# Kernel tuning notes

Hardware: AMD Instinct MI355X
Metric: run time of the kernel (lower is better)

## Reference

```python
import jax, jax.numpy as jnp
import numpy as np

C = 256
NUM_HEADS = 8
GROUPS = 8
EPS = 1e-5


def setup_inputs() -> dict:
    key = jax.random.key(0)
    ks = jax.random.split(key, 7)
    B, H, W = 2, 64, 64
    x = jax.random.normal(ks[0], (B, C, H, W), dtype=jnp.float32)
    gn_weight = jnp.ones((C,), dtype=jnp.float32)
    gn_bias = jnp.zeros((C,), dtype=jnp.float32)
    # 1x1 convs == per-pixel linear layers
    w_qkv = jax.random.normal(ks[1], (3 * C, C), dtype=jnp.float32) * (1.0 / np.sqrt(C))
    b_qkv = jax.random.normal(ks[2], (3 * C,), dtype=jnp.float32) * 0.01
    w_proj = jax.random.normal(ks[3], (C, C), dtype=jnp.float32) * (1.0 / np.sqrt(C))
    b_proj = jax.random.normal(ks[4], (C,), dtype=jnp.float32) * 0.01
    return {"x": x, "gn_weight": gn_weight, "gn_bias": gn_bias,
            "w_qkv": w_qkv, "b_qkv": b_qkv, "w_proj": w_proj, "b_proj": b_proj}


def reference(x, gn_weight, gn_bias, w_qkv, b_qkv, w_proj, b_proj):
    B, Cc, H, W = x.shape
    nh = NUM_HEADS
    hd = Cc // nh
    N = H * W
    scale = hd ** (-0.5)

    # GroupNorm(8, C): normalize over (C/G, H, W) per group, biased variance
    xg = x.reshape(B, GROUPS, Cc // GROUPS, H, W)
    mean = xg.mean(axis=(2, 3, 4), keepdims=True)
    var = xg.var(axis=(2, 3, 4), keepdims=True)
    hn = (xg - mean) * jax.lax.rsqrt(var + EPS)
    hn = hn.reshape(B, Cc, H, W) * gn_weight[None, :, None, None] + gn_bias[None, :, None, None]

    hf = hn.reshape(B, Cc, N)                       # [B, C, N]
    qkv = jnp.einsum('oc,bcn->bon', w_qkv, hf) + b_qkv[None, :, None]  # [B, 3C, N]
    qkv = qkv.reshape(B, 3, nh, hd, N)
    # q,k,v: [B, nh, N, hd]
    q = jnp.transpose(qkv[:, 0], (0, 1, 3, 2))
    k = jnp.transpose(qkv[:, 1], (0, 1, 3, 2))
    v = jnp.transpose(qkv[:, 2], (0, 1, 3, 2))

    attn = jnp.einsum('bhqd,bhkd->bhqk', q, k) * scale  # [B, nh, N, N]
    attn = jax.nn.softmax(attn, axis=-1)
    o = jnp.einsum('bhqk,bhkd->bhqd', attn, v)           # [B, nh, N, hd]
    o = jnp.transpose(o, (0, 1, 3, 2)).reshape(B, Cc, H, W)

    of = o.reshape(B, Cc, N)
    out = jnp.einsum('oc,bcn->bon', w_proj, of) + b_proj[None, :, None]
    return out.reshape(B, Cc, H, W)
```

## Files before the change

kernel.cpp:

```cpp
#include <hip/hip_runtime.h>


typedef _Float16 half8 __attribute__((ext_vector_type(8)));
typedef __fp16   fp16x2 __attribute__((ext_vector_type(2)));
typedef float    f32x4 __attribute__((ext_vector_type(4)));
typedef int      int2v __attribute__((ext_vector_type(2)));
typedef int      int4v __attribute__((ext_vector_type(4)));

__device__ __forceinline__ f32x4 mfma16(half8 a, half8 b, f32x4 c) {
  return __builtin_amdgcn_mfma_f32_16x16x32_f16(a, b, c, 0, 0, 0);
}

#if __has_builtin(__builtin_amdgcn_exp2f)
#define EXP2(x) __builtin_amdgcn_exp2f(x)
#else
#define EXP2(x) exp2f(x)
#endif

__device__ __forceinline__ unsigned short h_bits(_Float16 h) {
  return __builtin_bit_cast(unsigned short, h);
}
__device__ __forceinline__ int h2_bits(fp16x2 h) {
  return __builtin_bit_cast(int, h);
}

constexpr float CSCALE = (float)(1.4426950408889634 / 5.656854249492381);
constexpr float VSCALE = 0.0009765625f;
constexpr float VUNSC  = 1024.0f;

__global__ __launch_bounds__(256) void prep(const float* __restrict__ x,
                                            float* __restrict__ stats,
                                            const float* __restrict__ wq,
                                            const float* __restrict__ wp,
                                            _Float16* __restrict__ wqh,
                                            _Float16* __restrict__ wph) {
  const int tid = threadIdx.x;
  if (blockIdx.x < 512) {
    const int bg = blockIdx.x >> 5, ch = blockIdx.x & 31;
    const float* p = x + (size_t)bg * 131072 + (size_t)ch * 4096;
    float s = 0.f, ss = 0.f;
#pragma unroll
    for (int j = 0; j < 4; ++j) {
      f32x4 v = *(const f32x4*)(p + j * 1024 + tid * 4);
#pragma unroll
      for (int k = 0; k < 4; ++k) { s += v[k]; ss += v[k] * v[k]; }
    }
#pragma unroll
    for (int m = 1; m <= 32; m <<= 1) { s += __shfl_xor(s, m); ss += __shfl_xor(ss, m); }
    __shared__ float red[8];
    const int wv = tid >> 6;
    if ((tid & 63) == 0) { red[wv * 2] = s; red[wv * 2 + 1] = ss; }
    __syncthreads();
    if (tid == 0) {
      float S = red[0] + red[2] + red[4] + red[6];
      float SS = red[1] + red[3] + red[5] + red[7];
      atomicAdd(&stats[bg * 2], S);
      atomicAdd(&stats[bg * 2 + 1], SS);
    }
  } else {
    const int idx = (blockIdx.x - 512) * 256 + tid;
    if (idx < 196608) {
      wqh[idx] = (_Float16)wq[idx];
    } else {
      wph[idx - 196608] = (_Float16)wp[idx - 196608];
    }
  }
}

__global__ __launch_bounds__(256) void gn_apply(const float* __restrict__ x,
                                                const float* __restrict__ gw,
                                                const float* __restrict__ gb,
                                                const float* __restrict__ stats,
                                                _Float16* __restrict__ hn) {
  __shared__ float tile[64 * 65];
  const int tid = threadIdx.x;
  const int a = tid & 15;
  const int row16 = tid >> 4;
  const int b = blockIdx.z, c0 = blockIdx.y * 64, n0 = blockIdx.x * 64;
#pragma unroll
  for (int m = 0; m < 4; ++m) {
    const int cl = row16 + 16 * m;
    const int c = c0 + cl;
    const int g = c >> 5;
    const float s = stats[(b * 8 + g) * 2];
    const float ss = stats[(b * 8 + g) * 2 + 1];
    const float mean = s * (1.f / 131072.f);
    const float var = ss * (1.f / 131072.f) - mean * mean;
    const float rstd = rsqrtf(var + 1e-5f);
    const float ga = gw[c] * rstd;
    const float be = gb[c] - mean * ga;
    f32x4 xv = *(const f32x4*)(x + ((size_t)(b * 256 + c)) * 4096 + n0 + a * 4);
#pragma unroll
    for (int j = 0; j < 4; ++j) tile[cl * 65 + a * 4 + j] = xv[j] * ga + be;
  }
  __syncthreads();
#pragma unroll
  for (int m = 0; m < 4; ++m) {
    const int nl = row16 + 16 * m;
    const int cb = a * 4;
    int2v uh;
    unsigned short hh[4];
#pragma unroll
    for (int j = 0; j < 4; ++j) {
      hh[j] = h_bits((_Float16)tile[(cb + j) * 65 + nl]);
    }
    uh[0] = hh[0] | (hh[1] << 16); uh[1] = hh[2] | (hh[3] << 16);
    size_t off = ((size_t)(b * 4096 + n0 + nl)) * 256 + c0 + cb;
    *(int2v*)(hn + off) = uh;
  }
}

template <int MODE>
__global__ __launch_bounds__(256) void gemm_f16(
    const _Float16* __restrict__ W, const _Float16* __restrict__ Bm,
    const float* __restrict__ bias,
    _Float16* __restrict__ qkT, _Float16* __restrict__ v_t,
    float* __restrict__ outp) {
  __shared__ _Float16 a_lds[2][4096];
  __shared__ _Float16 b_lds[2][4096];
  const int tid = threadIdx.x, lane = tid & 63, wv = tid >> 6;
  const int qq = lane >> 4, ii = lane & 15;
  const int m0 = blockIdx.x * 64, n0 = blockIdx.y * 64, bz = blockIdx.z;

  const _Float16* asrc[2];
  const _Float16* bsrc[2];
  int dst8[2];
#pragma unroll
  for (int rep = 0; rep < 2; ++rep) {
    const int idx = tid + 256 * rep;
    dst8[rep] = idx * 8;
    const int j = idx >> 7, c = (idx >> 6) & 1, l = idx & 63;
    const int lq = l >> 4, li = l & 15;
    asrc[rep] = W + (size_t)(m0 + 16 * j + li) * 256 + 32 * c + 8 * lq;
    bsrc[rep] = Bm + ((size_t)(bz * 4096 + n0 + 16 * j + li)) * 256 + 32 * c + 8 * lq;
  }

  f32x4 acc[4] = {};

  half8 ar0 = *(const half8*)asrc[0];
  half8 ar1 = *(const half8*)asrc[1];
  half8 br0 = *(const half8*)bsrc[0];
  half8 br1 = *(const half8*)bsrc[1];
  *(half8*)(a_lds[0] + dst8[0]) = ar0;
  *(half8*)(a_lds[0] + dst8[1]) = ar1;
  *(half8*)(b_lds[0] + dst8[0]) = br0;
  *(half8*)(b_lds[0] + dst8[1]) = br1;
  __syncthreads();

  for (int it = 0; it < 4; ++it) {
    const int cur = it & 1;
    if (it < 3) {
      const int ko = (it + 1) * 64;
      ar0 = *(const half8*)(asrc[0] + ko);
      ar1 = *(const half8*)(asrc[1] + ko);
      br0 = *(const half8*)(bsrc[0] + ko);
      br1 = *(const half8*)(bsrc[1] + ko);
    }
    half8 ah0 = *(const half8*)(a_lds[cur] + ((wv * 2 + 0) * 64 + lane) * 8);
    half8 ah1 = *(const half8*)(a_lds[cur] + ((wv * 2 + 1) * 64 + lane) * 8);
#pragma unroll
    for (int t = 0; t < 4; ++t) {
      half8 b0 = *(const half8*)(b_lds[cur] + ((t * 2 + 0) * 64 + lane) * 8);
      half8 b1 = *(const half8*)(b_lds[cur] + ((t * 2 + 1) * 64 + lane) * 8);
      acc[t] = mfma16(ah0, b0, acc[t]);
      acc[t] = mfma16(ah1, b1, acc[t]);
    }
    if (it < 3) {
      _Float16* an = a_lds[cur ^ 1];
      _Float16* bn = b_lds[cur ^ 1];
      *(half8*)(an + dst8[0]) = ar0;
      *(half8*)(an + dst8[1]) = ar1;
      *(half8*)(bn + dst8[0]) = br0;
      *(half8*)(bn + dst8[1]) = br1;
    }
    __syncthreads();
  }

  const int och0 = m0 + 16 * wv + 4 * qq;
  if (MODE == 0) {
    if (m0 < 512) {
      const float sc = (m0 < 256) ? CSCALE : 1.0f;
#pragma unroll
      for (int t = 0; t < 4; ++t) {
        const int n = n0 + 16 * t + ii;
        unsigned short hh[4];
#pragma unroll
        for (int r = 0; r < 4; ++r) {
          hh[r] = h_bits((_Float16)((acc[t][r] + bias[och0 + r]) * sc));
        }
        int2v u;
        u[0] = hh[0] | (hh[1] << 16);
        u[1] = hh[2] | (hh[3] << 16);
        *(int2v*)(qkT + ((size_t)(bz * 4096 + n)) * 512 + och0) = u;
      }
    } else {
#pragma unroll
      for (int t = 0; t < 4; ++t) {
#pragma unroll
        for (int r = 0; r < 4; ++r) {
          const int och = och0 + r;
          const int d = och - 512;
          const int hd_ = d & 31, head = d >> 5;
          const int n = n0 + 16 * t + ii;
          v_t[((size_t)((bz * 8 + head) * 32 + hd_)) * 4096 + n] =
              (_Float16)((acc[t][r] + bias[och]) * VSCALE);
        }
      }
    }
  } else {
#pragma unroll
    for (int t = 0; t < 4; ++t) {
#pragma unroll
      for (int r = 0; r < 4; ++r) {
        const int och = och0 + r;
        const int n = n0 + 16 * t + ii;
        outp[((size_t)(bz * 256 + och)) * 4096 + n] = acc[t][r] + bias[och];
      }
    }
  }
}

__global__ __launch_bounds__(256, 8) void attn_kernel(
    const _Float16* __restrict__ qkT, const _Float16* __restrict__ v_t,
    _Float16* __restrict__ opart, float* __restrict__ lpart, int pbase) {
  __shared__ _Float16 k_lds[2][2048];
  __shared__ _Float16 v_lds[2][2048];
  const int tid = threadIdx.x, lane = tid & 63, wv = tid >> 6;
  const int qq = lane >> 4, ii = lane & 15;
  const int bh = blockIdx.y, b = bh >> 3, h = bh & 7;
  const int n0 = blockIdx.x * 128;
  const int part = pbase + blockIdx.z;
  const int key0 = part * 512;

  const _Float16* qbase =
      qkT + ((size_t)(b * 4096 + n0 + 32 * wv + ii)) * 512 + h * 32 + 8 * qq;
  half8 qf0 = *(const half8*)qbase;
  half8 qf1 = *(const half8*)(qbase + (size_t)16 * 512);

  const int f = tid >> 6, l = tid & 63;
  const int fq = l >> 4, fi = l & 15;
  const int u0 = f >> 1, hf = f & 1;
  const int g = 32 * u0 + 4 * hf + 8 * (fi >> 2) + (fi & 3);
  const _Float16* ksrc =
      qkT + ((size_t)(b * 4096 + key0 + g)) * 512 + 256 + h * 32 + 8 * fq;
  const _Float16* vsrc =
      v_t + ((size_t)(bh * 32 + 16 * hf + fi)) * 4096 + key0 + 32 * u0 + 8 * fq;
  const int dst8 = tid * 8;

  half8 ones8;
#pragma unroll
  for (int j = 0; j < 8; ++j) ones8[j] = (_Float16)1.0f;

  f32x4 o00 = {}, o10 = {}, o01 = {}, o11 = {}, accl0 = {}, accl1 = {};

  half8 kr = *(const half8*)ksrc;
  half8 vr = *(const half8*)vsrc;
  *(half8*)(k_lds[0] + dst8) = kr;
  *(half8*)(v_lds[0] + dst8) = vr;
  __syncthreads();

  for (int kb = 0; kb < 8; ++kb) {
    const int cur = kb & 1;
    if (kb < 7) {
      kr = *(const half8*)(ksrc + (size_t)(kb + 1) * 64 * 512);
      vr = *(const half8*)(vsrc + (size_t)(kb + 1) * 64);
    }
    const _Float16* kbase = k_lds[cur];
    const _Float16* vbase = v_lds[cur];

#pragma unroll
    for (int u = 0; u < 2; ++u) {
      half8 kfa = *(const half8*)(kbase + u * 1024 + lane * 8);
      half8 kfb = *(const half8*)(kbase + u * 1024 + 512 + lane * 8);
      f32x4 z = {};
      f32x4 sa0 = mfma16(kfa, qf0, z);
      f32x4 sb0 = mfma16(kfb, qf0, z);
      f32x4 sa1 = mfma16(kfa, qf1, z);
      f32x4 sb1 = mfma16(kfb, qf1, z);
      int4v p0, p1;
      p0[0] = h2_bits(__builtin_amdgcn_cvt_pkrtz(EXP2(sa0[0]), EXP2(sa0[1])));
      p0[1] = h2_bits(__builtin_amdgcn_cvt_pkrtz(EXP2(sa0[2]), EXP2(sa0[3])));
      p0[2] = h2_bits(__builtin_amdgcn_cvt_pkrtz(EXP2(sb0[0]), EXP2(sb0[1])));
      p0[3] = h2_bits(__builtin_amdgcn_cvt_pkrtz(EXP2(sb0[2]), EXP2(sb0[3])));
      p1[0] = h2_bits(__builtin_amdgcn_cvt_pkrtz(EXP2(sa1[0]), EXP2(sa1[1])));
      p1[1] = h2_bits(__builtin_amdgcn_cvt_pkrtz(EXP2(sa1[2]), EXP2(sa1[3])));
      p1[2] = h2_bits(__builtin_amdgcn_cvt_pkrtz(EXP2(sb1[0]), EXP2(sb1[1])));
      p1[3] = h2_bits(__builtin_amdgcn_cvt_pkrtz(EXP2(sb1[2]), EXP2(sb1[3])));
      half8 pt0 = __builtin_bit_cast(half8, p0);
      half8 pt1 = __builtin_bit_cast(half8, p1);
      half8 vf0 = *(const half8*)(vbase + u * 1024 + lane * 8);
      half8 vf1 = *(const half8*)(vbase + u * 1024 + 512 + lane * 8);
      o00 = mfma16(vf0, pt0, o00);
      o10 = mfma16(vf1, pt0, o10);
      accl0 = mfma16(ones8, pt0, accl0);
      o01 = mfma16(vf0, pt1, o01);
      o11 = mfma16(vf1, pt1, o11);
      accl1 = mfma16(ones8, pt1, accl1);
    }

    if (kb < 7) {
      *(half8*)(k_lds[cur ^ 1] + dst8) = kr;
      *(half8*)(v_lds[cur ^ 1] + dst8) = vr;
    }
    __syncthreads();
  }

#pragma unroll
  for (int hfq = 0; hfq < 2; ++hfq) {
    const f32x4 oa = hfq ? o01 : o00;
    const f32x4 ob = hfq ? o11 : o10;
    const int q = n0 + 32 * wv + 16 * hfq + ii;
    _Float16* base =
        opart + ((size_t)((part * 2 + b) * 4096 + q)) * 256 + h * 32;
    unsigned short hh[4];
    int2v ua;
#pragma unroll
    for (int r = 0; r < 4; ++r) hh[r] = h_bits((_Float16)oa[r]);
    ua[0] = hh[0] | (hh[1] << 16); ua[1] = hh[2] | (hh[3] << 16);
    *(int2v*)(base + 4 * qq) = ua;
#pragma unroll
    for (int r = 0; r < 4; ++r) hh[r] = h_bits((_Float16)ob[r]);
    ua[0] = hh[0] | (hh[1] << 16); ua[1] = hh[2] | (hh[3] << 16);
    *(int2v*)(base + 16 + 4 * qq) = ua;
    if (qq == 0) {
      lpart[((size_t)((part * 2 + b) * 4096 + q)) * 8 + h] =
          hfq ? accl1[0] : accl0[0];
    }
  }
}

__global__ __launch_bounds__(256) void attn_combine(
    const _Float16* __restrict__ opart, const float* __restrict__ lpart,
    _Float16* __restrict__ o16) {
  const int c = threadIdx.x, hh = c >> 5;
#pragma unroll
  for (int k = 0; k < 4; ++k) {
    const int row = blockIdx.x * 4 + k;
    const int b = row >> 12, q = row & 4095;
    float O = 0.f, L = 0.f;
#pragma unroll
    for (int p = 0; p < 8; ++p) {
      O += (float)opart[((size_t)((p * 2 + b) * 4096 + q)) * 256 + c];
      L += lpart[((size_t)((p * 2 + b) * 4096 + q)) * 8 + hh];
    }
    o16[(size_t)row * 256 + c] = (_Float16)(O * (VUNSC / L));
  }
}

extern "C" void kernel_launch(void* const* d_in, const int* in_sizes, int n_in,
                              void* d_out, int out_size, void* d_ws, size_t ws_size,
                              hipStream_t stream) {
  const float* x     = (const float*)d_in[0];
  const float* gnw   = (const float*)d_in[1];
  const float* gnb   = (const float*)d_in[2];
  const float* wqkv  = (const float*)d_in[3];
  const float* bqkv  = (const float*)d_in[4];
  const float* wproj = (const float*)d_in[5];
  const float* bproj = (const float*)d_in[6];
  float* out = (float*)d_out;

  char* ws = (char*)d_ws;
  size_t off = 0;
  auto alloc = [&](size_t bytes) -> char* {
    char* p = ws + off;
    off += (bytes + 255) & ~(size_t)255;
    return p;
  };
  float*    stats  = (float*)alloc(128);
  _Float16* hn     = (_Float16*)alloc((size_t)2 * 4096 * 256 * 2);
  _Float16* wq_h   = (_Float16*)alloc((size_t)768 * 256 * 2);
  _Float16* wp_h   = (_Float16*)alloc((size_t)256 * 256 * 2);
  _Float16* qkT    = (_Float16*)alloc((size_t)2 * 4096 * 512 * 2);
  _Float16* v_t    = (_Float16*)alloc((size_t)16 * 32 * 4096 * 2);
  _Float16* opart  = (_Float16*)alloc((size_t)16 * 4096 * 256 * 2);
  float*    lpart  = (float*)alloc((size_t)16 * 4096 * 8 * 4);
  _Float16* o16 = hn;
  if (off > ws_size) return;

  (void)hipMemsetAsync(stats, 0, 256, stream);
  prep<<<1536, 256, 0, stream>>>(x, stats, wqkv, wproj, wq_h, wp_h);
  gn_apply<<<dim3(64, 4, 2), 256, 0, stream>>>(x, gnw, gnb, stats, hn);
  gemm_f16<0><<<dim3(12, 64, 2), 256, 0, stream>>>(wq_h, hn, bqkv, qkT, v_t,
                                                   nullptr);
  attn_kernel<<<dim3(32, 16, 4), 256, 0, stream>>>(qkT, v_t, opart, lpart, 0);
  attn_kernel<<<dim3(32, 16, 4), 256, 0, stream>>>(qkT, v_t, opart, lpart, 4);
  attn_combine<<<2048, 256, 0, stream>>>(opart, lpart, o16);
  gemm_f16<1><<<dim3(4, 64, 2), 256, 0, stream>>>(wp_h, o16, bproj, nullptr,
                                                  nullptr, out);
}
```

Before: 185.6 us.

## Halve attention key splits and fuse partial combine into projection GEMM

The attention key split goes from 8 partitions of 512 keys over two launches to 4 partitions of 1024 keys in one launch, which halves the partial-output traffic. The separate combine kernel is replaced by a tiny kernel that reduces row sums to inverse normalisers. The projection GEMM now sums the 4 fp16 partials and scales them while staging its B operand. This removes one launch and one full intermediate write and read, at the cost of longer attention blocks, fewer concurrent blocks, and partial summation done in fp16.

```diff
diff --git a/kernel.cpp b/kernel.cpp
--- a/kernel.cpp
+++ b/kernel.cpp
@@ -110,12 +110,10 @@
   }
 }
 
-template <int MODE>
-__global__ __launch_bounds__(256) void gemm_f16(
+__global__ __launch_bounds__(256) void gemm_qkv(
     const _Float16* __restrict__ W, const _Float16* __restrict__ Bm,
     const float* __restrict__ bias,
-    _Float16* __restrict__ qkT, _Float16* __restrict__ v_t,
-    float* __restrict__ outp) {
+    _Float16* __restrict__ qkT, _Float16* __restrict__ v_t) {
   __shared__ _Float16 a_lds[2][4096];
   __shared__ _Float16 b_lds[2][4096];
   const int tid = threadIdx.x, lane = tid & 63, wv = tid >> 6;
@@ -177,35 +175,20 @@
   }
 
   const int och0 = m0 + 16 * wv + 4 * qq;
-  if (MODE == 0) {
-    if (m0 < 512) {
-      const float sc = (m0 < 256) ? CSCALE : 1.0f;
-#pragma unroll
-      for (int t = 0; t < 4; ++t) {
-        const int n = n0 + 16 * t + ii;
-        unsigned short hh[4];
-#pragma unroll
-        for (int r = 0; r < 4; ++r) {
-          hh[r] = h_bits((_Float16)((acc[t][r] + bias[och0 + r]) * sc));
-        }
-        int2v u;
-        u[0] = hh[0] | (hh[1] << 16);
-        u[1] = hh[2] | (hh[3] << 16);
-        *(int2v*)(qkT + ((size_t)(bz * 4096 + n)) * 512 + och0) = u;
+  if (m0 < 512) {
+    const float sc = (m0 < 256) ? CSCALE : 1.0f;
+#pragma unroll
+    for (int t = 0; t < 4; ++t) {
+      const int n = n0 + 16 * t + ii;
+      unsigned short hh[4];
+#pragma unroll
+      for (int r = 0; r < 4; ++r) {
+        hh[r] = h_bits((_Float16)((acc[t][r] + bias[och0 + r]) * sc));
       }
-    } else {
-#pragma unroll
-      for (int t = 0; t < 4; ++t) {
-#pragma unroll
-        for (int r = 0; r < 4; ++r) {
-          const int och = och0 + r;
-          const int d = och - 512;
-          const int hd_ = d & 31, head = d >> 5;
-          const int n = n0 + 16 * t + ii;
-          v_t[((size_t)((bz * 8 + head) * 32 + hd_)) * 4096 + n] =
-              (_Float16)((acc[t][r] + bias[och]) * VSCALE);
-        }
-      }
+      int2v u;
+      u[0] = hh[0] | (hh[1] << 16);
+      u[1] = hh[2] | (hh[3] << 16);
+      *(int2v*)(qkT + ((size_t)(bz * 4096 + n)) * 512 + och0) = u;
     }
   } else {
 #pragma unroll
@@ -213,8 +196,11 @@
 #pragma unroll
       for (int r = 0; r < 4; ++r) {
         const int och = och0 + r;
+        const int d = och - 512;
+        const int hd_ = d & 31, head = d >> 5;
         const int n = n0 + 16 * t + ii;
-        outp[((size_t)(bz * 256 + och)) * 4096 + n] = acc[t][r] + bias[och];
+        v_t[((size_t)((bz * 8 + head) * 32 + hd_)) * 4096 + n] =
+            (_Float16)((acc[t][r] + bias[och]) * VSCALE);
       }
     }
   }
@@ -222,15 +208,15 @@
 
 __global__ __launch_bounds__(256, 8) void attn_kernel(
     const _Float16* __restrict__ qkT, const _Float16* __restrict__ v_t,
-    _Float16* __restrict__ opart, float* __restrict__ lpart, int pbase) {
+    _Float16* __restrict__ opart, float* __restrict__ lpart) {
   __shared__ _Float16 k_lds[2][2048];
   __shared__ _Float16 v_lds[2][2048];
   const int tid = threadIdx.x, lane = tid & 63, wv = tid >> 6;
   const int qq = lane >> 4, ii = lane & 15;
   const int bh = blockIdx.y, b = bh >> 3, h = bh & 7;
   const int n0 = blockIdx.x * 128;
-  const int part = pbase + blockIdx.z;
-  const int key0 = part * 512;
+  const int part = blockIdx.z;
+  const int key0 = part * 1024;
 
   const _Float16* qbase =
       qkT + ((size_t)(b * 4096 + n0 + 32 * wv + ii)) * 512 + h * 32 + 8 * qq;
@@ -259,9 +245,9 @@
   *(half8*)(v_lds[0] + dst8) = vr;
   __syncthreads();
 
-  for (int kb = 0; kb < 8; ++kb) {
+  for (int kb = 0; kb < 16; ++kb) {
     const int cur = kb & 1;
-    if (kb < 7) {
+    if (kb < 15) {
       kr = *(const half8*)(ksrc + (size_t)(kb + 1) * 64 * 512);
       vr = *(const half8*)(vsrc + (size_t)(kb + 1) * 64);
     }
@@ -298,7 +284,7 @@
       accl1 = mfma16(ones8, pt1, accl1);
     }
 
-    if (kb < 7) {
+    if (kb < 15) {
       *(half8*)(k_lds[cur ^ 1] + dst8) = kr;
       *(half8*)(v_lds[cur ^ 1] + dst8) = vr;
     }
@@ -329,21 +315,103 @@
   }
 }
 
-__global__ __launch_bounds__(256) void attn_combine(
-    const _Float16* __restrict__ opart, const float* __restrict__ lpart,
-    _Float16* __restrict__ o16) {
-  const int c = threadIdx.x, hh = c >> 5;
-#pragma unroll
-  for (int k = 0; k < 4; ++k) {
-    const int row = blockIdx.x * 4 + k;
-    const int b = row >> 12, q = row & 4095;
-    float O = 0.f, L = 0.f;
-#pragma unroll
-    for (int p = 0; p < 8; ++p) {
-      O += (float)opart[((size_t)((p * 2 + b) * 4096 + q)) * 256 + c];
-      L += lpart[((size_t)((p * 2 + b) * 4096 + q)) * 8 + hh];
-    }
-    o16[(size_t)row * 256 + c] = (_Float16)(O * (VUNSC / L));
+__global__ __launch_bounds__(256) void lsum(const float* __restrict__ lpart,
+                                            float* __restrict__ linv) {
+  const int i = blockIdx.x * 256 + threadIdx.x;
+  float L = lpart[i] + lpart[i + 65536] + lpart[i + 131072] + lpart[i + 196608];
+  linv[i] = VUNSC / L;
+}
+
+__global__ __launch_bounds__(256) void gemm_proj(
+    const _Float16* __restrict__ W, const _Float16* __restrict__ opart,
+    const float* __restrict__ linv, const float* __restrict__ bias,
+    float* __restrict__ outp) {
+  __shared__ _Float16 a_lds[2][4096];
+  __shared__ _Float16 b_lds[2][4096];
+  const int tid = threadIdx.x, lane = tid & 63, wv = tid >> 6;
+  const int qq = lane >> 4, ii = lane & 15;
+  const int m0 = blockIdx.x * 64, n0 = blockIdx.y * 64, bz = blockIdx.z;
+  const size_t PSTR = (size_t)2 * 4096 * 256;
+
+  const _Float16* asrc[2];
+  const _Float16* bsrc[2];
+  int dst8[2], li_idx[2], cch[2];
+#pragma unroll
+  for (int rep = 0; rep < 2; ++rep) {
+    const int idx = tid + 256 * rep;
+    dst8[rep] = idx * 8;
+    const int j = idx >> 7, c = (idx >> 6) & 1, l = idx & 63;
+    const int lq = l >> 4, li = l & 15;
+    const int q = n0 + 16 * j + li;
+    asrc[rep] = W + (size_t)(m0 + 16 * j + li) * 256 + 32 * c + 8 * lq;
+    bsrc[rep] = opart + ((size_t)(bz * 4096 + q)) * 256 + 32 * c + 8 * lq;
+    li_idx[rep] = (bz * 4096 + q) * 8 + c;
+    cch[rep] = c;
+  }
+
+  f32x4 acc[4] = {};
+
+  auto stage_b = [&](int rep, int ko, int it) -> half8 {
+    const _Float16* p = bsrc[rep] + ko;
+    half8 s0 = *(const half8*)p;
+    half8 s1 = *(const half8*)(p + PSTR);
+    half8 s2 = *(const half8*)(p + 2 * PSTR);
+    half8 s3 = *(const half8*)(p + 3 * PSTR);
+    half8 s = (s0 + s1) + (s2 + s3);
+    const _Float16 invh = (_Float16)linv[li_idx[rep] + 2 * it];
+#pragma unroll
+    for (int j = 0; j < 8; ++j) s[j] *= invh;
+    return s;
+  };
+
+  half8 ar0 = *(const half8*)asrc[0];
+  half8 ar1 = *(const half8*)asrc[1];
+  half8 br0 = stage_b(0, 0, 0);
+  half8 br1 = stage_b(1, 0, 0);
+  *(half8*)(a_lds[0] + dst8[0]) = ar0;
+  *(half8*)(a_lds[0] + dst8[1]) = ar1;
+  *(half8*)(b_lds[0] + dst8[0]) = br0;
+  *(half8*)(b_lds[0] + dst8[1]) = br1;
+  __syncthreads();
+
+  for (int it = 0; it < 4; ++it) {
+    const int cur = it & 1;
+    if (it < 3) {
+      const int ko = (it + 1) * 64;
+      ar0 = *(const half8*)(asrc[0] + ko);
+      ar1 = *(const half8*)(asrc[1] + ko);
+      br0 = stage_b(0, ko, it + 1);
+      br1 = stage_b(1, ko, it + 1);
+    }
+    half8 ah0 = *(const half8*)(a_lds[cur] + ((wv * 2 + 0) * 64 + lane) * 8);
+    half8 ah1 = *(const half8*)(a_lds[cur] + ((wv * 2 + 1) * 64 + lane) * 8);
+#pragma unroll
+    for (int t = 0; t < 4; ++t) {
+      half8 b0 = *(const half8*)(b_lds[cur] + ((t * 2 + 0) * 64 + lane) * 8);
+      half8 b1 = *(const half8*)(b_lds[cur] + ((t * 2 + 1) * 64 + lane) * 8);
+      acc[t] = mfma16(ah0, b0, acc[t]);
+      acc[t] = mfma16(ah1, b1, acc[t]);
+    }
+    if (it < 3) {
+      _Float16* an = a_lds[cur ^ 1];
+      _Float16* bn = b_lds[cur ^ 1];
+      *(half8*)(an + dst8[0]) = ar0;
+      *(half8*)(an + dst8[1]) = ar1;
+      *(half8*)(bn + dst8[0]) = br0;
+      *(half8*)(bn + dst8[1]) = br1;
+    }
+    __syncthreads();
+  }
+
+  const int och0 = m0 + 16 * wv + 4 * qq;
+#pragma unroll
+  for (int t = 0; t < 4; ++t) {
+#pragma unroll
+    for (int r = 0; r < 4; ++r) {
+      const int och = och0 + r;
+      const int n = n0 + 16 * t + ii;
+      outp[((size_t)(bz * 256 + och)) * 4096 + n] = acc[t][r] + bias[och];
+    }
   }
 }
 
@@ -372,19 +440,16 @@
   _Float16* wp_h   = (_Float16*)alloc((size_t)256 * 256 * 2);
   _Float16* qkT    = (_Float16*)alloc((size_t)2 * 4096 * 512 * 2);
   _Float16* v_t    = (_Float16*)alloc((size_t)16 * 32 * 4096 * 2);
-  _Float16* opart  = (_Float16*)alloc((size_t)16 * 4096 * 256 * 2);
-  float*    lpart  = (float*)alloc((size_t)16 * 4096 * 8 * 4);
-  _Float16* o16 = hn;
+  _Float16* opart  = (_Float16*)alloc((size_t)8 * 4096 * 256 * 2);
+  float*    lpart  = (float*)alloc((size_t)8 * 4096 * 8 * 4);
+  float*    linv   = (float*)alloc((size_t)2 * 4096 * 8 * 4);
   if (off > ws_size) return;
 
   (void)hipMemsetAsync(stats, 0, 256, stream);
   prep<<<1536, 256, 0, stream>>>(x, stats, wqkv, wproj, wq_h, wp_h);
   gn_apply<<<dim3(64, 4, 2), 256, 0, stream>>>(x, gnw, gnb, stats, hn);
-  gemm_f16<0><<<dim3(12, 64, 2), 256, 0, stream>>>(wq_h, hn, bqkv, qkT, v_t,
-                                                   nullptr);
-  attn_kernel<<<dim3(32, 16, 4), 256, 0, stream>>>(qkT, v_t, opart, lpart, 0);
-  attn_kernel<<<dim3(32, 16, 4), 256, 0, stream>>>(qkT, v_t, opart, lpart, 4);
-  attn_combine<<<2048, 256, 0, stream>>>(opart, lpart, o16);
-  gemm_f16<1><<<dim3(4, 64, 2), 256, 0, stream>>>(wp_h, o16, bproj, nullptr,
-                                                  nullptr, out);
-}
+  gemm_qkv<<<dim3(12, 64, 2), 256, 0, stream>>>(wq_h, hn, bqkv, qkT, v_t);
+  attn_kernel<<<dim3(32, 16, 4), 256, 0, stream>>>(qkT, v_t, opart, lpart);
+  lsum<<<256, 256, 0, stream>>>(lpart, linv);
+  gemm_proj<<<dim3(4, 64, 2), 256, 0, stream>>>(wp_h, opart, linv, bproj, out);
+}
```

After: 172.6 us. -7.0%, faster.
